# Kernel tuning notes

Hardware: AMD Instinct MI355X
Metric: run time of the kernel (lower is better)

Reference implementation:

```python
import jax, jax.numpy as jnp
import numpy as np
from jax import lax

BATCH, C, HH, WW = 4, 3, 512, 512


def _dark_min(x, patch):
    # min over channels, reflect-pad, min over patch x patch window (torch unfold+min)
    pad = (patch - 1) // 2
    m = jnp.min(x, axis=1, keepdims=True)                      # [B,1,H,W]
    m = jnp.pad(m, ((0, 0), (0, 0), (pad, pad), (pad, pad)), mode='reflect')
    return lax.reduce_window(m, jnp.array(jnp.inf, m.dtype), lax.min,
                             (1, 1, patch, patch), (1, 1, 1, 1), 'VALID')


def _soft_thresh(x, lam):
    return jnp.sign(x) * jnp.maximum(jnp.abs(x) - lam, 0.0)


def _conv3x3(x, w):
    return lax.conv_general_dilated(x, w, (1, 1), 'SAME',
                                    dimension_numbers=('NCHW', 'OIHW', 'NCHW'))


def setup_inputs() -> dict:
    key = jax.random.key(0)
    names = ['I', 't_p', 'B_p', 'B', 't', 'J', 'G', 'H', 'P', 'Q', 'u', 'v', 'X', 'Y']
    keys = jax.random.split(key, len(names) + 2)
    inp = {n: jax.random.uniform(keys[i], (BATCH, C, HH, WW), dtype=jnp.float32)
           for i, n in enumerate(names)}
    for g in ['gamma_1', 'gamma_2', 'gamma_3', 'gamma_4', 'gamma_5']:
        inp[g] = jnp.array([3.001], dtype=jnp.float32)
    inp['t1d_w'] = jax.random.normal(keys[-2], (1, 3, 1, 1), dtype=jnp.float32) * 0.3
    inp['hnet_w'] = jax.random.normal(keys[-1], (3, 3, 3, 3), dtype=jnp.float32) * 0.1
    inp['patch_size'] = 35
    return inp


def _forward(I, t_p, B_p, B, t, J, G, H, P, Q, u, v, X, Y,
             gamma_1, gamma_2, gamma_3, gamma_4, gamma_5, t1d_w, hnet_w, patch_size):
    lam1, lam2, lam3, lam4, lam5 = 1.0, 0.7, 0.3, 1.0, 1.0

    # ---- get_mean_value + mapping_index (vectorized over batch) ----
    mean = jnp.mean(J, axis=(2, 3))                 # [B,3]
    idx = jnp.argsort(mean, axis=1)                 # ascending, like torch.sort
    ms = jnp.take_along_axis(mean, idx, axis=1)     # sorted means
    gather = lambda k: jnp.take_along_axis(J, idx[:, k][:, None, None, None], axis=1)
    J_l, J_m, J_s = gather(2), gather(1), gather(0)           # [B,1,H,W]
    bar = lambda k: ms[:, k][:, None, None, None]
    J_m = J_m + (bar(2) - bar(1)) * J_l
    J_s = J_s + (bar(2) - bar(0)) * J_l
    ch = jnp.arange(3)[None, :]                     # scatter channels back
    J = jnp.where((ch == idx[:, 1:2])[:, :, None, None], J_m, J)
    J = jnp.where((ch == idx[:, 0:1])[:, :, None, None], J_s, J)

    # ---- B update (spatial mean broadcast back) ----
    Bn = (lam3 * B_p - lam1 * (J * t - I) * (1.0 - t)) / (lam1 * (1.0 - t) ** 2 + lam3)
    Bn = jnp.mean(Bn, axis=(2, 3), keepdims=True) * jnp.ones_like(I)

    # ---- t update + 1x1 conv + channel replicate ----
    tn = (lam2 * t_p + gamma_4 * H - lam1 * (Bn - I) * (J - Bn) - X) / \
         (lam1 * (J - Bn) ** 2 + lam2 + gamma_4)
    t1 = jnp.einsum('oc,bchw->bohw', t1d_w[:, :, 0, 0], tn)   # [B,1,H,W]
    tn = jnp.concatenate([t1, t1, t1], axis=1)

    # ---- J, u, v updates ----
    Jn = (lam1 * (tn * (I - Bn * (1.0 - tn))) + gamma_3 * G + gamma_4 * u
          - gamma_5 * v - Y + gamma_5) / (lam1 * tn * tn + gamma_3 + gamma_4 + gamma_5)
    un = (gamma_1 * u + gamma_4 * Jn) / (gamma_1 + gamma_4)
    vn = (gamma_2 * v - gamma_5 * Jn + gamma_5) / (gamma_2 + gamma_5)

    # ---- H_Net (conv stand-in for RDN), dual updates ----
    Hn = _conv3x3(tn + X / gamma_4, hnet_w)
    Xn = X + gamma_4 * (tn - Hn)
    Yn = Y + gamma_3 * (Jn - G)

    # ---- dark channel + soft threshold ----
    M_u = _dark_min(un, patch_size)
    M_v = _dark_min(vn, patch_size)
    Pn = _soft_thresh(M_u, lam4 / gamma_1)
    Qn = _soft_thresh(M_v, lam5 / gamma_1)

    return (Bn, tn, Jn, G, Hn, Pn, Qn, un, vn, Xn, Yn, gamma_3)


def reference(I, t_p, B_p, B, t, J, G, H, P, Q, u, v, X, Y,
              gamma_1, gamma_2, gamma_3, gamma_4, gamma_5, t1d_w, hnet_w, patch_size):
    return _forward(I, t_p, B_p, B, t, J, G, H, P, Q, u, v, X, Y,
                    gamma_1, gamma_2, gamma_3, gamma_4, gamma_5, t1d_w, hnet_w, patch_size)
```

## Files before the change

kernel.cpp:

```cpp
#include <hip/hip_runtime.h>
#include <math.h>

#define W_ 512
#define H_ 512
#define HW_ 262144
#define HW4_ 65536
#define CHW_ 786432

#define O_Bn 0
#define O_tn 3145728
#define O_Jn 6291456
#define O_G  9437184
#define O_Hn 12582912
#define O_Pn 15728640
#define O_Qn 16777216
#define O_un 17825792
#define O_vn 20971520
#define O_Xn 24117248
#define O_Yn 27262976
#define O_g3 30408704

#define LAM2 0.7f
#define LAM3 0.3f

__global__ __launch_bounds__(256) void kRed(const float* __restrict__ J,
                                            const float* __restrict__ tt,
                                            const float* __restrict__ B_p,
                                            const float* __restrict__ I,
                                            float* __restrict__ sums) {
    int blk = blockIdx.x;
    int b = blk >> 7, chunk = blk & 127;
    size_t pb = (size_t)b * (CHW_ / 4);
    size_t cb = (size_t)chunk * 512;
    const float4* J4 = (const float4*)J;
    const float4* t4 = (const float4*)tt;
    const float4* B4 = (const float4*)B_p;
    const float4* I4 = (const float4*)I;

    float aJ[3] = {0.f, 0.f, 0.f};
    float a1[3] = {0.f, 0.f, 0.f};
    float a2[9] = {0.f, 0.f, 0.f, 0.f, 0.f, 0.f, 0.f, 0.f, 0.f};

    #pragma unroll
    for (int k = 0; k < 2; ++k) {
        size_t o = cb + threadIdx.x + k * 256;
        float4 j0 = J4[pb + 0 * HW4_ + o];
        float4 j1 = J4[pb + 1 * HW4_ + o];
        float4 j2 = J4[pb + 2 * HW4_ + o];
        #pragma unroll
        for (int c = 0; c < 3; ++c) {
            float4 tv = t4[pb + (size_t)c * HW4_ + o];
            float4 bp = B4[pb + (size_t)c * HW4_ + o];
            float4 iv = I4[pb + (size_t)c * HW4_ + o];
            float4 jc = (c == 0) ? j0 : (c == 1 ? j1 : j2);
#define REDC(m) { \
            float omt = 1.f - tv.m; \
            float r = 1.f / (omt * omt + LAM3); \
            float g = tv.m * omt * r; \
            aJ[c] += jc.m; \
            a1[c] += (LAM3 * bp.m - (jc.m * tv.m - iv.m) * omt) * r; \
            a2[0 * 3 + c] += j0.m * g; \
            a2[1 * 3 + c] += j1.m * g; \
            a2[2 * 3 + c] += j2.m * g; }
            REDC(x) REDC(y) REDC(z) REDC(w)
#undef REDC
        }
    }

    float vals[15];
    #pragma unroll
    for (int c = 0; c < 3; ++c) { vals[c] = aJ[c]; vals[3 + c] = a1[c]; }
    #pragma unroll
    for (int s = 0; s < 9; ++s) vals[6 + s] = a2[s];

    __shared__ float lds[4][15];
    int lane = threadIdx.x & 63, w = threadIdx.x >> 6;
    #pragma unroll
    for (int s = 0; s < 15; ++s) {
        float v = vals[s];
        #pragma unroll
        for (int off = 32; off; off >>= 1) v += __shfl_down(v, off, 64);
        if (lane == 0) lds[w][s] = v;
    }
    __syncthreads();
    if (threadIdx.x < 15) {
        int s = threadIdx.x;
        sums[blk * 16 + s] = lds[0][s] + lds[1][s] + lds[2][s] + lds[3][s];
    }
}

__global__ void kFin(const float* __restrict__ sums,
                     float* __restrict__ alpha, int* __restrict__ idx2,
                     float* __restrict__ BnS,
                     const float* __restrict__ g3p, float* __restrict__ outg3) {
    __shared__ float tot[4][15];
    int t = threadIdx.x;
    if (t < 60) {
        int b = t / 15, s = t % 15;
        const float* p = sums + (size_t)b * 128 * 16 + s;
        float acc = 0.f;
        for (int ch = 0; ch < 128; ++ch) acc += p[ch * 16];
        tot[b][s] = acc;
    }
    __syncthreads();
    if (t < 4) {
        const float invHW = 1.0f / (float)HW_;
        float m[3] = {tot[t][0] * invHW, tot[t][1] * invHW, tot[t][2] * invHW};
        int r[3];
        #pragma unroll
        for (int i = 0; i < 3; ++i) {
            int ri = 0;
            #pragma unroll
            for (int j = 0; j < 3; ++j)
                if (j != i && (m[j] < m[i] || (m[j] == m[i] && j < i))) ri++;
            r[i] = ri;
        }
        int idx[3]; float ms[3];
        #pragma unroll
        for (int i = 0; i < 3; ++i) { idx[r[i]] = i; ms[r[i]] = m[i]; }
        idx2[t] = idx[2];
        float a[3] = {0.f, 0.f, 0.f};
        a[idx[1]] = ms[2] - ms[1];
        a[idx[0]] = ms[2] - ms[0];
        #pragma unroll
        for (int c = 0; c < 3; ++c) {
            alpha[t * 3 + c] = a[c];
            BnS[t * 3 + c] = (tot[t][3 + c] - a[c] * tot[t][6 + idx[2] * 3 + c]) * invHW;
        }
    }
    if (t == 0) *outg3 = g3p[0];
}

__global__ __launch_bounds__(256) void kMain(
    const float* __restrict__ I, const float* __restrict__ t_p,
    const float* __restrict__ Hm, const float* __restrict__ Xm,
    const float* __restrict__ J, const float* __restrict__ u,
    const float* __restrict__ v, const float* __restrict__ Y,
    const float* __restrict__ G,
    const float* __restrict__ g1p, const float* __restrict__ g2p,
    const float* __restrict__ g3p, const float* __restrict__ g4p,
    const float* __restrict__ g5p, const float* __restrict__ t1w,
    const float* __restrict__ alpha, const int* __restrict__ idx2,
    const float* __restrict__ BnS,
    float* __restrict__ out)
{
    int id = blockIdx.x * 256 + threadIdx.x;
    int b = id >> 16, q = id & (HW4_ - 1);
    float g1 = g1p[0], g2 = g2p[0], g3 = g3p[0], g4 = g4p[0], g5 = g5p[0];
    float wc[3] = {t1w[0], t1w[1], t1w[2]};
    int i2 = idx2[b];
    size_t pb = (size_t)b * (CHW_ / 4);
    const float4* I4p = (const float4*)I;
    const float4* tp4p = (const float4*)t_p;
    const float4* H4p = (const float4*)Hm;
    const float4* X4p = (const float4*)Xm;
    const float4* J4p = (const float4*)J;
    const float4* u4p = (const float4*)u;
    const float4* v4p = (const float4*)v;
    const float4* Y4p = (const float4*)Y;
    const float4* G4p = (const float4*)G;
    float4* o4 = (float4*)out;

    float4 Jl = J4p[pb + (size_t)i2 * HW4_ + q];
    float4 t1 = make_float4(0.f, 0.f, 0.f, 0.f);
    float4 Isv[3]; float Bsv[3];
    const float den2 = LAM2 + g4;
    #pragma unroll
    for (int c = 0; c < 3; ++c) {
        size_t o = pb + (size_t)c * HW4_ + q;
        float4 I4 = I4p[o], tp4 = tp4p[o], H4 = H4p[o], X4 = X4p[o], Jv = J4p[o];
        float al = alpha[b * 3 + c], Bnv = BnS[b * 3 + c];
        float wcc = wc[c];
#define STEP1(m) { \
        float d_ = (Jv.m + al * Jl.m) - Bnv; \
        float tnr_ = (LAM2 * tp4.m + g4 * H4.m - (Bnv - I4.m) * d_ - X4.m) / (d_ * d_ + den2); \
        t1.m += wcc * tnr_; }
        STEP1(x) STEP1(y) STEP1(z) STEP1(w)
#undef STEP1
        Isv[c] = I4; Bsv[c] = Bnv;
    }
    float g345 = g3 + g4 + g5;
    float4 invDen;
    invDen.x = 1.f / (t1.x * t1.x + g345);
    invDen.y = 1.f / (t1.y * t1.y + g345);
    invDen.z = 1.f / (t1.z * t1.z + g345);
    invDen.w = 1.f / (t1.w * t1.w + g345);
    float invDu = 1.f / (g1 + g4), invDv = 1.f / (g2 + g5);
    float4 cu = make_float4(1e30f, 1e30f, 1e30f, 1e30f);
    float4 cv = cu;
    #pragma unroll
    for (int c = 0; c < 3; ++c) {
        size_t o = pb + (size_t)c * HW4_ + q;
        float4 u4 = u4p[o], v4 = v4p[o], Y4 = Y4p[o], G4 = G4p[o];
        float Bnv = Bsv[c];
        float4 Jn4, un4, vn4, Yn4;
#define STEP2(m) { \
        float Jn_ = (t1.m * (Isv[c].m - Bnv * (1.f - t1.m)) + g3 * G4.m + g4 * u4.m \
                     - g5 * v4.m - Y4.m + g5) * invDen.m; \
        float un_ = (g1 * u4.m + g4 * Jn_) * invDu; \
        float vn_ = (g2 * v4.m - g5 * Jn_ + g5) * invDv; \
        Jn4.m = Jn_; un4.m = un_; vn4.m = vn_; \
        Yn4.m = Y4.m + g3 * (Jn_ - G4.m); \
        cu.m = fminf(cu.m, un_); cv.m = fminf(cv.m, vn_); }
        STEP2(x) STEP2(y) STEP2(z) STEP2(w)
#undef STEP2
        o4[O_Bn / 4 + o] = make_float4(Bnv, Bnv, Bnv, Bnv);
        o4[O_tn / 4 + o] = t1;
        o4[O_Jn / 4 + o] = Jn4;
        o4[O_G  / 4 + o] = G4;
        o4[O_un / 4 + o] = un4;
        o4[O_vn / 4 + o] = vn4;
        o4[O_Yn / 4 + o] = Yn4;
    }
    o4[O_Pn / 4 + (size_t)b * HW4_ + q] = cu;
    o4[O_Qn / 4 + (size_t)b * HW4_ + q] = cv;
}

__global__ __launch_bounds__(256) void kHMin(float* __restrict__ out) {
    __shared__ float row[546];
    int blk = blockIdx.x;
    int tensor = blk >> 11;
    int rem = blk & 2047;
    int b = rem >> 9, y = rem & 511;
    const float* src = out + (tensor ? O_Qn : O_Pn) + b * HW_ + y * W_;
    float* dst = out + (tensor ? O_Xn : O_Hn) + b * HW_ + y * W_;
    for (int j = threadIdx.x; j < 546; j += 256) {
        int xx = j - 17;
        xx = xx < 0 ? -xx : (xx >= W_ ? 2 * W_ - 2 - xx : xx);
        row[j] = src[xx];
    }
    __syncthreads();
    for (int x = threadIdx.x; x < W_; x += 256) {
        float m = row[x];
        #pragma unroll
        for (int k = 1; k < 35; ++k) m = fminf(m, row[x + k]);
        dst[x] = m;
    }
}

__global__ __launch_bounds__(256) void kVMin(const float* __restrict__ g1p,
                                             float* __restrict__ out) {
    int tensor = blockIdx.x >> 12;
    int lid = ((blockIdx.x & 4095) << 8) + threadIdx.x;
    int b = lid >> 18, p = lid & (HW_ - 1);
    int y = p >> 9, x = p & 511;
    const float* R = out + (tensor ? O_Xn : O_Hn) + b * HW_;
    float m = 1e30f;
    #pragma unroll
    for (int k = 0; k < 35; ++k) {
        int yy = y + k - 17;
        yy = yy < 0 ? -yy : (yy >= H_ ? 2 * H_ - 2 - yy : yy);
        m = fminf(m, R[yy * W_ + x]);
    }
    float lam = 1.0f / g1p[0];
    float s = (m > 0.f) ? 1.f : (m < 0.f ? -1.f : 0.f);
    float r = s * fmaxf(fabsf(m) - lam, 0.f);
    out[(tensor ? O_Qn : O_Pn) + b * HW_ + p] = r;
}

__global__ __launch_bounds__(256) void kConv(const float* __restrict__ Xm,
                                             const float* __restrict__ hw,
                                             const float* __restrict__ g4p,
                                             float* __restrict__ out) {
    __shared__ float w[81];
    if (threadIdx.x < 81) w[threadIdx.x] = hw[threadIdx.x];
    __syncthreads();
    int id = blockIdx.x * 256 + threadIdx.x;
    int b = id >> 18, p = id & (HW_ - 1);
    int y = p >> 9, x = p & 511;
    float g4 = g4p[0], ig4 = 1.f / g4;
    const float* tn = out + O_tn + (size_t)b * CHW_;
    float acc0 = 0.f, acc1 = 0.f, acc2 = 0.f;
    #pragma unroll
    for (int ky = 0; ky < 3; ++ky) {
        int yy = y + ky - 1;
        if (yy < 0 || yy >= H_) continue;
        #pragma unroll
        for (int kx = 0; kx < 3; ++kx) {
            int xx = x + kx - 1;
            if (xx < 0 || xx >= W_) continue;
            int pp = yy * W_ + xx;
            float t1v = tn[pp];
            #pragma unroll
            for (int i = 0; i < 3; ++i) {
                float Av = t1v + Xm[(size_t)(b * 3 + i) * HW_ + pp] * ig4;
                int kk = i * 9 + ky * 3 + kx;
                acc0 += w[kk] * Av;
                acc1 += w[27 + kk] * Av;
                acc2 += w[54 + kk] * Av;
            }
        }
    }
    float t1c = tn[p];
    float acc[3] = {acc0, acc1, acc2};
    #pragma unroll
    for (int o = 0; o < 3; ++o) {
        size_t oo = (size_t)(b * 3 + o) * HW_ + p;
        out[O_Hn + oo] = acc[o];
        out[O_Xn + oo] = Xm[oo] + g4 * (t1c - acc[o]);
    }
}

extern "C" void kernel_launch(void* const* d_in, const int* in_sizes, int n_in,
                              void* d_out, int out_size, void* d_ws, size_t ws_size,
                              hipStream_t stream) {
    (void)in_sizes; (void)n_in; (void)out_size; (void)ws_size;
    const float* I   = (const float*)d_in[0];
    const float* t_p = (const float*)d_in[1];
    const float* B_p = (const float*)d_in[2];
    const float* tt  = (const float*)d_in[4];
    const float* J   = (const float*)d_in[5];
    const float* G   = (const float*)d_in[6];
    const float* Hm  = (const float*)d_in[7];
    const float* u   = (const float*)d_in[10];
    const float* v   = (const float*)d_in[11];
    const float* X   = (const float*)d_in[12];
    const float* Y   = (const float*)d_in[13];
    const float* g1  = (const float*)d_in[14];
    const float* g2  = (const float*)d_in[15];
    const float* g3  = (const float*)d_in[16];
    const float* g4  = (const float*)d_in[17];
    const float* g5  = (const float*)d_in[18];
    const float* t1w = (const float*)d_in[19];
    const float* hw  = (const float*)d_in[20];
    float* out = (float*)d_out;
    float* ws  = (float*)d_ws;

    float* sums  = ws;
    float* alpha = ws + 8192;
    int*   idx2  = (int*)(ws + 8204);
    float* BnS   = ws + 8208;

    kRed<<<512, 256, 0, stream>>>(J, tt, B_p, I, sums);
    kFin<<<1, 64, 0, stream>>>(sums, alpha, idx2, BnS, g3, out + O_g3);
    kMain<<<1024, 256, 0, stream>>>(I, t_p, Hm, X, J, u, v, Y, G,
                                    g1, g2, g3, g4, g5, t1w, alpha, idx2, BnS, out);
    kHMin<<<4096, 256, 0, stream>>>(out);
    kVMin<<<8192, 256, 0, stream>>>(g1, out);
    kConv<<<4096, 256, 0, stream>>>(X, hw, g4, out);
}
```

Before: 329.2 us.

## Fuse vertical min and conv into one launch, add non-temporal stores

The horizontal-min intermediate now goes to a workspace scratch buffer instead of the Hn/Xn output regions. That removes the dependency that forced the vertical-min and conv kernels to run in sequence, so the two are merged into one kernel split by block index and run concurrently. Bulk output writes in kMain and the tail use non-temporal stores to reduce cache pollution. kFin is widened to 256 threads, with four lanes reducing each partial sum. The scratch needs 8 MB of workspace, and non-temporal stores could hurt if tn or other outputs are re-read soon.

```diff
diff --git a/kernel.cpp b/kernel.cpp
--- a/kernel.cpp
+++ b/kernel.cpp
@@ -22,6 +22,19 @@
 
 #define LAM2 0.7f
 #define LAM3 0.3f
+
+#define WS_SUMS   0
+#define WS_ALPHA  8192
+#define WS_IDX2   8204
+#define WS_BNS    8208
+#define WS_SCR    16384
+
+typedef float nfloat4 __attribute__((ext_vector_type(4)));
+
+__device__ __forceinline__ void nt_store4(float4 v, float4* p) {
+    nfloat4 nv; nv.x = v.x; nv.y = v.y; nv.z = v.z; nv.w = v.w;
+    __builtin_nontemporal_store(nv, (nfloat4*)p);
+}
 
 __global__ __launch_bounds__(256) void kRed(const float* __restrict__ J,
                                             const float* __restrict__ tt,
@@ -89,18 +102,25 @@
     }
 }
 
-__global__ void kFin(const float* __restrict__ sums,
+__global__ __launch_bounds__(256) void kFin(const float* __restrict__ sums,
                      float* __restrict__ alpha, int* __restrict__ idx2,
                      float* __restrict__ BnS,
                      const float* __restrict__ g3p, float* __restrict__ outg3) {
+    __shared__ float part[64][4];
     __shared__ float tot[4][15];
     int t = threadIdx.x;
-    if (t < 60) {
-        int b = t / 15, s = t % 15;
+    int g = t >> 2, sub = t & 3;
+    if (g < 60) {
+        int b = g / 15, s = g % 15;
         const float* p = sums + (size_t)b * 128 * 16 + s;
         float acc = 0.f;
-        for (int ch = 0; ch < 128; ++ch) acc += p[ch * 16];
-        tot[b][s] = acc;
+        #pragma unroll 8
+        for (int ch = sub; ch < 128; ch += 4) acc += p[ch * 16];
+        part[g][sub] = acc;
+    }
+    __syncthreads();
+    if (t < 60) {
+        tot[t / 15][t % 15] = (part[t][0] + part[t][1]) + (part[t][2] + part[t][3]);
     }
     __syncthreads();
     if (t < 4) {
@@ -204,26 +224,27 @@
         cu.m = fminf(cu.m, un_); cv.m = fminf(cv.m, vn_); }
         STEP2(x) STEP2(y) STEP2(z) STEP2(w)
 #undef STEP2
-        o4[O_Bn / 4 + o] = make_float4(Bnv, Bnv, Bnv, Bnv);
+        nt_store4(make_float4(Bnv, Bnv, Bnv, Bnv), &o4[O_Bn / 4 + o]);
         o4[O_tn / 4 + o] = t1;
-        o4[O_Jn / 4 + o] = Jn4;
-        o4[O_G  / 4 + o] = G4;
-        o4[O_un / 4 + o] = un4;
-        o4[O_vn / 4 + o] = vn4;
-        o4[O_Yn / 4 + o] = Yn4;
+        nt_store4(Jn4, &o4[O_Jn / 4 + o]);
+        nt_store4(G4,  &o4[O_G  / 4 + o]);
+        nt_store4(un4, &o4[O_un / 4 + o]);
+        nt_store4(vn4, &o4[O_vn / 4 + o]);
+        nt_store4(Yn4, &o4[O_Yn / 4 + o]);
     }
     o4[O_Pn / 4 + (size_t)b * HW4_ + q] = cu;
     o4[O_Qn / 4 + (size_t)b * HW4_ + q] = cv;
 }
 
-__global__ __launch_bounds__(256) void kHMin(float* __restrict__ out) {
+__global__ __launch_bounds__(256) void kHMin(const float* __restrict__ out,
+                                             float* __restrict__ scr) {
     __shared__ float row[546];
     int blk = blockIdx.x;
     int tensor = blk >> 11;
     int rem = blk & 2047;
     int b = rem >> 9, y = rem & 511;
     const float* src = out + (tensor ? O_Qn : O_Pn) + b * HW_ + y * W_;
-    float* dst = out + (tensor ? O_Xn : O_Hn) + b * HW_ + y * W_;
+    float* dst = scr + (size_t)(tensor * 4 + b) * HW_ + y * W_;
     for (int j = threadIdx.x; j < 546; j += 256) {
         int xx = j - 17;
         xx = xx < 0 ? -xx : (xx >= W_ ? 2 * W_ - 2 - xx : xx);
@@ -238,66 +259,67 @@
     }
 }
 
-__global__ __launch_bounds__(256) void kVMin(const float* __restrict__ g1p,
-                                             float* __restrict__ out) {
-    int tensor = blockIdx.x >> 12;
-    int lid = ((blockIdx.x & 4095) << 8) + threadIdx.x;
-    int b = lid >> 18, p = lid & (HW_ - 1);
-    int y = p >> 9, x = p & 511;
-    const float* R = out + (tensor ? O_Xn : O_Hn) + b * HW_;
-    float m = 1e30f;
-    #pragma unroll
-    for (int k = 0; k < 35; ++k) {
-        int yy = y + k - 17;
-        yy = yy < 0 ? -yy : (yy >= H_ ? 2 * H_ - 2 - yy : yy);
-        m = fminf(m, R[yy * W_ + x]);
-    }
-    float lam = 1.0f / g1p[0];
-    float s = (m > 0.f) ? 1.f : (m < 0.f ? -1.f : 0.f);
-    float r = s * fmaxf(fabsf(m) - lam, 0.f);
-    out[(tensor ? O_Qn : O_Pn) + b * HW_ + p] = r;
-}
-
-__global__ __launch_bounds__(256) void kConv(const float* __restrict__ Xm,
+__global__ __launch_bounds__(256) void kTail(const float* __restrict__ scr,
+                                             const float* __restrict__ Xm,
                                              const float* __restrict__ hw,
+                                             const float* __restrict__ g1p,
                                              const float* __restrict__ g4p,
                                              float* __restrict__ out) {
     __shared__ float w[81];
-    if (threadIdx.x < 81) w[threadIdx.x] = hw[threadIdx.x];
-    __syncthreads();
-    int id = blockIdx.x * 256 + threadIdx.x;
-    int b = id >> 18, p = id & (HW_ - 1);
-    int y = p >> 9, x = p & 511;
-    float g4 = g4p[0], ig4 = 1.f / g4;
-    const float* tn = out + O_tn + (size_t)b * CHW_;
-    float acc0 = 0.f, acc1 = 0.f, acc2 = 0.f;
-    #pragma unroll
-    for (int ky = 0; ky < 3; ++ky) {
-        int yy = y + ky - 1;
-        if (yy < 0 || yy >= H_) continue;
-        #pragma unroll
-        for (int kx = 0; kx < 3; ++kx) {
-            int xx = x + kx - 1;
-            if (xx < 0 || xx >= W_) continue;
-            int pp = yy * W_ + xx;
-            float t1v = tn[pp];
+    if (blockIdx.x < 8192) {
+        int tensor = blockIdx.x >> 12;
+        int lid = ((blockIdx.x & 4095) << 8) + threadIdx.x;
+        int b = lid >> 18, p = lid & (HW_ - 1);
+        int y = p >> 9, x = p & 511;
+        const float* R = scr + (size_t)(tensor * 4 + b) * HW_;
+        float m = 1e30f;
+        #pragma unroll
+        for (int k = 0; k < 35; ++k) {
+            int yy = y + k - 17;
+            yy = yy < 0 ? -yy : (yy >= H_ ? 2 * H_ - 2 - yy : yy);
+            m = fminf(m, R[yy * W_ + x]);
+        }
+        float lam = 1.0f / g1p[0];
+        float s = (m > 0.f) ? 1.f : (m < 0.f ? -1.f : 0.f);
+        float r = s * fmaxf(fabsf(m) - lam, 0.f);
+        __builtin_nontemporal_store(r, &out[(tensor ? O_Qn : O_Pn) + b * HW_ + p]);
+    } else {
+        if (threadIdx.x < 81) w[threadIdx.x] = hw[threadIdx.x];
+        __syncthreads();
+        int id = (blockIdx.x - 8192) * 256 + threadIdx.x;
+        int b = id >> 18, p = id & (HW_ - 1);
+        int y = p >> 9, x = p & 511;
+        float g4 = g4p[0], ig4 = 1.f / g4;
+        const float* tn = out + O_tn + (size_t)b * CHW_;
+        float acc0 = 0.f, acc1 = 0.f, acc2 = 0.f;
+        #pragma unroll
+        for (int ky = 0; ky < 3; ++ky) {
+            int yy = y + ky - 1;
+            if (yy < 0 || yy >= H_) continue;
             #pragma unroll
-            for (int i = 0; i < 3; ++i) {
-                float Av = t1v + Xm[(size_t)(b * 3 + i) * HW_ + pp] * ig4;
-                int kk = i * 9 + ky * 3 + kx;
-                acc0 += w[kk] * Av;
-                acc1 += w[27 + kk] * Av;
-                acc2 += w[54 + kk] * Av;
+            for (int kx = 0; kx < 3; ++kx) {
+                int xx = x + kx - 1;
+                if (xx < 0 || xx >= W_) continue;
+                int pp = yy * W_ + xx;
+                float t1v = tn[pp];
+                #pragma unroll
+                for (int i = 0; i < 3; ++i) {
+                    float Av = t1v + Xm[(size_t)(b * 3 + i) * HW_ + pp] * ig4;
+                    int kk = i * 9 + ky * 3 + kx;
+                    acc0 += w[kk] * Av;
+                    acc1 += w[27 + kk] * Av;
+                    acc2 += w[54 + kk] * Av;
+                }
             }
         }
-    }
-    float t1c = tn[p];
-    float acc[3] = {acc0, acc1, acc2};
-    #pragma unroll
-    for (int o = 0; o < 3; ++o) {
-        size_t oo = (size_t)(b * 3 + o) * HW_ + p;
-        out[O_Hn + oo] = acc[o];
-        out[O_Xn + oo] = Xm[oo] + g4 * (t1c - acc[o]);
+        float t1c = tn[p];
+        float acc[3] = {acc0, acc1, acc2};
+        #pragma unroll
+        for (int o = 0; o < 3; ++o) {
+            size_t oo = (size_t)(b * 3 + o) * HW_ + p;
+            __builtin_nontemporal_store(acc[o], &out[O_Hn + oo]);
+            __builtin_nontemporal_store(Xm[oo] + g4 * (t1c - acc[o]), &out[O_Xn + oo]);
+        }
     }
 }
 
@@ -326,16 +348,16 @@
     float* out = (float*)d_out;
     float* ws  = (float*)d_ws;
 
-    float* sums  = ws;
-    float* alpha = ws + 8192;
-    int*   idx2  = (int*)(ws + 8204);
-    float* BnS   = ws + 8208;
+    float* sums  = ws + WS_SUMS;
+    float* alpha = ws + WS_ALPHA;
+    int*   idx2  = (int*)(ws + WS_IDX2);
+    float* BnS   = ws + WS_BNS;
+    float* scr   = ws + WS_SCR;
 
     kRed<<<512, 256, 0, stream>>>(J, tt, B_p, I, sums);
-    kFin<<<1, 64, 0, stream>>>(sums, alpha, idx2, BnS, g3, out + O_g3);
+    kFin<<<1, 256, 0, stream>>>(sums, alpha, idx2, BnS, g3, out + O_g3);
     kMain<<<1024, 256, 0, stream>>>(I, t_p, Hm, X, J, u, v, Y, G,
                                     g1, g2, g3, g4, g5, t1w, alpha, idx2, BnS, out);
-    kHMin<<<4096, 256, 0, stream>>>(out);
-    kVMin<<<8192, 256, 0, stream>>>(g1, out);
-    kConv<<<4096, 256, 0, stream>>>(X, hw, g4, out);
-}
+    kHMin<<<4096, 256, 0, stream>>>(out, scr);
+    kTail<<<12288, 256, 0, stream>>>(scr, X, hw, g1, g4, out);
+}
```

After: 322.7 us. 2.0% less time.
